# Performance work log

Measured on AMD Instinct MI355X. Metric: run time of the kernel, lower is better.

Reference implementation:

```python
import jax, jax.numpy as jnp
import numpy as np

N_NODES = 100000
N_EDGES = 1600000
C_IN, C_HID, C_OUT = 64, 64, 32


def _gcn_conv(x, src, dst, ew, W, b, n_nodes):
    """PyG GCNConv: add self-loops (weight 1), symmetric normalization,
    out[dst] += norm * (x @ W)[src], plus bias. Dropout omitted (eval mode)."""
    h = x @ W  # [N, C_out_layer]
    loop = jnp.arange(n_nodes, dtype=src.dtype)
    src_a = jnp.concatenate([src, loop])
    dst_a = jnp.concatenate([dst, loop])
    ew_a = jnp.concatenate([ew, jnp.ones((n_nodes,), dtype=ew.dtype)])
    # degree over incoming (dst) side, weighted
    deg = jax.ops.segment_sum(ew_a, dst_a, num_segments=n_nodes)
    dinv = jnp.where(deg > 0, jax.lax.rsqrt(deg), 0.0)
    norm = dinv[src_a] * ew_a * dinv[dst_a]  # [E+N]
    msg = h[src_a] * norm[:, None]           # gather + scale: [E+N, C]
    out = jax.ops.segment_sum(msg, dst_a, num_segments=n_nodes)  # scatter-add
    return out + b


def setup_inputs() -> dict:
    key = jax.random.key(0)
    k1, k2, k3, k4, k5, k6, k7 = jax.random.split(key, 7)
    x = jax.random.normal(k1, (N_NODES, C_IN), dtype=jnp.float32)
    edge_index = jax.random.randint(k2, (2, N_EDGES), 0, N_NODES, dtype=jnp.int64)
    edge_attr = jax.random.uniform(k3, (N_EDGES,), dtype=jnp.float32)
    s1 = 1.0 / np.sqrt(C_IN)
    s2 = 1.0 / np.sqrt(C_HID)
    W1 = jax.random.uniform(k4, (C_IN, C_HID), jnp.float32, -s1, s1)
    b1 = jnp.zeros((C_HID,), dtype=jnp.float32)
    W2 = jax.random.uniform(k5, (C_HID, C_OUT), jnp.float32, -s2, s2)
    b2 = jnp.zeros((C_OUT,), dtype=jnp.float32)
    return {"x": x, "edge_index": edge_index, "edge_attr": edge_attr,
            "W1": W1, "b1": b1, "W2": W2, "b2": b2}


def reference(x, edge_index, edge_attr, W1, b1, W2, b2):
    n = x.shape[0]
    src, dst = edge_index[0], edge_index[1]
    h = _gcn_conv(x, src, dst, edge_attr, W1, b1, n)
    h = jax.nn.relu(h)  # dropout is identity in eval mode
    out = _gcn_conv(h, src, dst, edge_attr, W2, b2, n)
    return out
```

## Files before the change

### kernel.cpp

```cpp
#include <hip/hip_runtime.h>
#include <hip/hip_fp16.h>


#define TPB 256
#define TPB_P 512
#define TPB_S 1024
#define BSH2 8
#define BN2 256
#define NBC 512
#define PCHUNK 4096
#define CAP2 5632
#define XSTR 68

typedef union { uint2 u; __half2 h[2]; } hpack;
typedef union { uint4 u; __half2 h[4]; } hpack8;

__device__ __forceinline__ int enc_w(float w) {
  unsigned b = __float_as_uint(w);
  return (int)(((b + 0x7FFFu + ((b >> 16) & 1u)) >> 16) & 0x7FFFu);
}
__device__ __forceinline__ float dec_w(int e) {
  return __uint_as_float(((unsigned)e >> 17) << 16);
}

__global__ __launch_bounds__(TPB_P) void k_fat(const int* __restrict__ si,
                                               const int* __restrict__ di,
                                               const float* __restrict__ ew,
                                               int* __restrict__ bpos,
                                               int2* __restrict__ tin,
                                               const float* __restrict__ x,
                                               const float* __restrict__ W1,
                                               __half* __restrict__ h1h,
                                               int e, int n, int gbp) {
  __shared__ union SM {
    struct {
      int hcnt[NBC]; int lst0[NBC]; int lcur[NBC]; int hbase[NBC];
      int wsum[8];
      int2 se[PCHUNK]; unsigned short sbk[PCHUNK];
    } p;
    float Wl[64 * 64];
  } sm;
  int t = threadIdx.x;
  if (blockIdx.x < (unsigned)gbp) {
    int lo = blockIdx.x * PCHUNK;
    int hi = lo + PCHUNK; if (hi > e) hi = e;
    int cn = hi - lo;
    sm.p.hcnt[t] = 0;
    __syncthreads();
    for (int i = lo + t; i < hi; i += TPB_P) atomicAdd(&sm.p.hcnt[di[i] >> BSH2], 1);
    __syncthreads();
    int c = sm.p.hcnt[t];
    int lane = t & 63, wid = t >> 6;
    int v = c;
#pragma unroll
    for (int off = 1; off < 64; off <<= 1) {
      int u = __shfl_up(v, off);
      if (lane >= off) v += u;
    }
    if (lane == 63) sm.p.wsum[wid] = v;
    __syncthreads();
    if (t < 64) {
      int s = (t < 8) ? sm.p.wsum[t] : 0;
#pragma unroll
      for (int off = 1; off < 8; off <<= 1) {
        int u = __shfl_up(s, off);
        if (t >= off) s += u;
      }
      if (t < 8) sm.p.wsum[t] = s;
    }
    __syncthreads();
    int incl = v + (wid ? sm.p.wsum[wid - 1] : 0);
    sm.p.hcnt[t] = incl;
    __syncthreads();
    {
      int bb = (t + blockIdx.x) & (NBC - 1);
      int inc = sm.p.hcnt[bb];
      int exc = bb ? sm.p.hcnt[bb - 1] : 0;
      int cb = inc - exc;
      sm.p.lst0[bb] = exc;
      sm.p.lcur[bb] = 0;
      sm.p.hbase[bb] = cb ? (bb * CAP2 + atomicAdd(&bpos[bb], cb)) : 0;
    }
    __syncthreads();
    for (int i = lo + t; i < hi; i += TPB_P) {
      int d = di[i];
      int bk = d >> BSH2;
      int loc = atomicAdd(&sm.p.lcur[bk], 1);
      int p = sm.p.lst0[bk] + loc;
      sm.p.se[p] = make_int2(si[i] | ((d & (BN2 - 1)) << 17), __float_as_int(ew[i]));
      sm.p.sbk[p] = (unsigned short)bk;
    }
    __syncthreads();
    for (int p = t; p < cn; p += TPB_P) {
      int bk = sm.p.sbk[p];
      tin[sm.p.hbase[bk] + (p - sm.p.lst0[bk])] = sm.p.se[p];
    }
  } else {
    {
      const float4* W4 = (const float4*)W1;
      float4* Wl4 = (float4*)sm.Wl;
#pragma unroll
      for (int i = 0; i < 2; ++i) Wl4[t + TPB_P * i] = W4[t + TPB_P * i];
    }
    __syncthreads();
    int r = (blockIdx.x - gbp) * 32 + (t >> 4);
    if (r >= n) return;
    int c0 = (t & 15) << 2;
    const float4* xr = (const float4*)(x + (size_t)r * 64);
    float ax = 0.f, ay = 0.f, az = 0.f, aw = 0.f;
#pragma unroll
    for (int kk = 0; kk < 16; ++kk) {
      float4 xv = xr[kk];
      const float* w = &sm.Wl[(kk * 4) * 64 + c0];
      float4 w0 = *(const float4*)(w);
      float4 w1 = *(const float4*)(w + 64);
      float4 w2 = *(const float4*)(w + 128);
      float4 w3 = *(const float4*)(w + 192);
      ax += xv.x * w0.x + xv.y * w1.x + xv.z * w2.x + xv.w * w3.x;
      ay += xv.x * w0.y + xv.y * w1.y + xv.z * w2.y + xv.w * w3.y;
      az += xv.x * w0.z + xv.y * w1.z + xv.z * w2.z + xv.w * w3.z;
      aw += xv.x * w0.w + xv.y * w1.w + xv.z * w2.w + xv.w * w3.w;
    }
    hpack pk;
    pk.h[0] = __floats2half2_rn(ax, ay);
    pk.h[1] = __floats2half2_rn(az, aw);
    *(uint2*)(h1h + (size_t)r * 64 + c0) = pk.u;
  }
}

__global__ __launch_bounds__(TPB_S) void k_sortb(const int2* __restrict__ tin,
                                                 const int* __restrict__ bpos,
                                                 int* __restrict__ colpk,
                                                 int2* __restrict__ rowseg,
                                                 float* __restrict__ dinv, int n) {
  __shared__ int cnt[BN2];
  __shared__ float degw[BN2];
  __shared__ int cur[BN2];
  __shared__ int ls[BN2];
  __shared__ int2 se[PCHUNK];
  int b = blockIdx.x, t = threadIdx.x;
  if (t < BN2) { cnt[t] = 0; degw[t] = 1.0f; }
  __syncthreads();
  int jb = b * CAP2, je = jb + bpos[b];
  for (int j = jb + t; j < je; j += TPB_S) {
    int2 p = tin[j];
    int o = j - jb;
    if (o < PCHUNK) se[o] = p;
    int dl = p.x >> 17;
    atomicAdd(&cnt[dl], 1);
    atomicAdd(&degw[dl], __int_as_float(p.y));
  }
  __syncthreads();
  int c = (t < BN2) ? cnt[t] : 0;
  int c4 = (c + 3) & ~3;
  if (t < BN2) ls[t] = c4;
  __syncthreads();
  for (int off = 1; off < BN2; off <<= 1) {
    int u = (t >= off && t < BN2) ? ls[t - off] : 0;
    __syncthreads();
    if (t < BN2) ls[t] += u;
    __syncthreads();
  }
  int base = b << BSH2;
  if (t < BN2) {
    int start = jb + ls[t] - c4;
    cur[t] = start;
    int node = base + t;
    if (node < n) {
      rowseg[node] = make_int2(start, start + c4);
      dinv[node] = rsqrtf(degw[t]);
    }
    for (int i = c; i < c4; ++i) colpk[start + i] = 0;
  }
  __syncthreads();
  for (int j = jb + t; j < je; j += TPB_S) {
    int o = j - jb;
    int2 p = (o < PCHUNK) ? se[o] : tin[j];
    int dl = p.x >> 17;
    int pos = atomicAdd(&cur[dl], 1);
    colpk[pos] = (p.x & 0x1FFFF) | (enc_w(__int_as_float(p.y)) << 17);
  }
}

__global__ __launch_bounds__(TPB) void k_gfuse(const __half* __restrict__ g1h,
                                               const int* __restrict__ colpk,
                                               const int2* __restrict__ rowseg,
                                               const float* __restrict__ dinv,
                                               const float* __restrict__ W2,
                                               const float* __restrict__ b1,
                                               __half* __restrict__ g2h, int n) {
  __shared__ float W2l[64 * 32];
  __shared__ float b1l[64];
  __shared__ float x2l[32 * XSTR];
  int t = threadIdx.x;
  {
    const float4* W4 = (const float4*)W2;
    float4* Wl4 = (float4*)W2l;
#pragma unroll
    for (int i = 0; i < 2; ++i) Wl4[t + TPB * i] = W4[t + TPB * i];
    if (t < 64) b1l[t] = b1[t];
  }
  __syncthreads();
  int node = t >> 3;
  int r = blockIdx.x * 32 + node;
  int c0 = (t & 7) << 3;
  bool valid = (r < n);
  float a[8];
  float dv = 0.f;
  if (valid) {
    dv = dinv[r];
    hpack8 s; s.u = *(const uint4*)(g1h + (size_t)r * 64 + c0);
#pragma unroll
    for (int k = 0; k < 4; ++k) {
      float2 f = __half22float2(s.h[k]);
      a[2 * k] = dv * f.x; a[2 * k + 1] = dv * f.y;
    }
    int2 seg = rowseg[r];
    int j = seg.x;
    for (; j + 7 < seg.y; j += 8) {
      int4 qa = *(const int4*)(colpk + j);
      int4 qb = *(const int4*)(colpk + j + 4);
      int s0 = qa.x & 0x1FFFF, s1 = qa.y & 0x1FFFF, s2 = qa.z & 0x1FFFF, s3 = qa.w & 0x1FFFF;
      int s4 = qb.x & 0x1FFFF, s5 = qb.y & 0x1FFFF, s6 = qb.z & 0x1FFFF, s7 = qb.w & 0x1FFFF;
      hpack8 u0; u0.u = *(const uint4*)(g1h + (size_t)s0 * 64 + c0);
      hpack8 u1; u1.u = *(const uint4*)(g1h + (size_t)s1 * 64 + c0);
      hpack8 u2; u2.u = *(const uint4*)(g1h + (size_t)s2 * 64 + c0);
      hpack8 u3; u3.u = *(const uint4*)(g1h + (size_t)s3 * 64 + c0);
      hpack8 u4; u4.u = *(const uint4*)(g1h + (size_t)s4 * 64 + c0);
      hpack8 u5; u5.u = *(const uint4*)(g1h + (size_t)s5 * 64 + c0);
      hpack8 u6; u6.u = *(const uint4*)(g1h + (size_t)s6 * 64 + c0);
      hpack8 u7; u7.u = *(const uint4*)(g1h + (size_t)s7 * 64 + c0);
      float w0 = dec_w(qa.x) * dinv[s0], w1 = dec_w(qa.y) * dinv[s1];
      float w2 = dec_w(qa.z) * dinv[s2], w3 = dec_w(qa.w) * dinv[s3];
      float w4 = dec_w(qb.x) * dinv[s4], w5 = dec_w(qb.y) * dinv[s5];
      float w6 = dec_w(qb.z) * dinv[s6], w7 = dec_w(qb.w) * dinv[s7];
#pragma unroll
      for (int k = 0; k < 4; ++k) {
        float2 f;
        f = __half22float2(u0.h[k]); a[2*k] += w0 * f.x; a[2*k+1] += w0 * f.y;
        f = __half22float2(u1.h[k]); a[2*k] += w1 * f.x; a[2*k+1] += w1 * f.y;
        f = __half22float2(u2.h[k]); a[2*k] += w2 * f.x; a[2*k+1] += w2 * f.y;
        f = __half22float2(u3.h[k]); a[2*k] += w3 * f.x; a[2*k+1] += w3 * f.y;
        f = __half22float2(u4.h[k]); a[2*k] += w4 * f.x; a[2*k+1] += w4 * f.y;
        f = __half22float2(u5.h[k]); a[2*k] += w5 * f.x; a[2*k+1] += w5 * f.y;
        f = __half22float2(u6.h[k]); a[2*k] += w6 * f.x; a[2*k+1] += w6 * f.y;
        f = __half22float2(u7.h[k]); a[2*k] += w7 * f.x; a[2*k+1] += w7 * f.y;
      }
    }
    if (j < seg.y) {
      int4 qa = *(const int4*)(colpk + j);
      int s0 = qa.x & 0x1FFFF, s1 = qa.y & 0x1FFFF, s2 = qa.z & 0x1FFFF, s3 = qa.w & 0x1FFFF;
      hpack8 u0; u0.u = *(const uint4*)(g1h + (size_t)s0 * 64 + c0);
      hpack8 u1; u1.u = *(const uint4*)(g1h + (size_t)s1 * 64 + c0);
      hpack8 u2; u2.u = *(const uint4*)(g1h + (size_t)s2 * 64 + c0);
      hpack8 u3; u3.u = *(const uint4*)(g1h + (size_t)s3 * 64 + c0);
      float w0 = dec_w(qa.x) * dinv[s0], w1 = dec_w(qa.y) * dinv[s1];
      float w2 = dec_w(qa.z) * dinv[s2], w3 = dec_w(qa.w) * dinv[s3];
#pragma unroll
      for (int k = 0; k < 4; ++k) {
        float2 f;
        f = __half22float2(u0.h[k]); a[2*k] += w0 * f.x; a[2*k+1] += w0 * f.y;
        f = __half22float2(u1.h[k]); a[2*k] += w1 * f.x; a[2*k+1] += w1 * f.y;
        f = __half22float2(u2.h[k]); a[2*k] += w2 * f.x; a[2*k+1] += w2 * f.y;
        f = __half22float2(u3.h[k]); a[2*k] += w3 * f.x; a[2*k+1] += w3 * f.y;
      }
    }
    float* xp = x2l + node * XSTR + c0;
#pragma unroll
    for (int k = 0; k < 8; k += 4) {
      float4 v = {fmaxf(dv * a[k + 0] + b1l[c0 + k + 0], 0.f),
                  fmaxf(dv * a[k + 1] + b1l[c0 + k + 1], 0.f),
                  fmaxf(dv * a[k + 2] + b1l[c0 + k + 2], 0.f),
                  fmaxf(dv * a[k + 3] + b1l[c0 + k + 3], 0.f)};
      *(float4*)(xp + k) = v;
    }
  }
  __syncthreads();
  if (!valid) return;
  int oc = (t & 7) << 2;
  const float* xr = x2l + node * XSTR;
  float ax = 0.f, ay = 0.f, az = 0.f, aw = 0.f;
#pragma unroll
  for (int kk = 0; kk < 16; ++kk) {
    float4 xv = *(const float4*)(xr + 4 * kk);
    const float* w = &W2l[(kk * 4) * 32 + oc];
    float4 w0 = *(const float4*)(w);
    float4 w1 = *(const float4*)(w + 32);
    float4 w2 = *(const float4*)(w + 64);
    float4 w3 = *(const float4*)(w + 96);
    ax += xv.x * w0.x + xv.y * w1.x + xv.z * w2.x + xv.w * w3.x;
    ay += xv.x * w0.y + xv.y * w1.y + xv.z * w2.y + xv.w * w3.y;
    az += xv.x * w0.z + xv.y * w1.z + xv.z * w2.z + xv.w * w3.z;
    aw += xv.x * w0.w + xv.y * w1.w + xv.z * w2.w + xv.w * w3.w;
  }
  hpack pk;
  pk.h[0] = __floats2half2_rn(ax, ay);
  pk.h[1] = __floats2half2_rn(az, aw);
  *(uint2*)(g2h + (size_t)r * 32 + oc) = pk.u;
}

__global__ __launch_bounds__(TPB) void k_gather32(const __half* __restrict__ g2h,
                                                  const int* __restrict__ colpk,
                                                  const int2* __restrict__ rowseg,
                                                  const float* __restrict__ dinv,
                                                  const float* __restrict__ b2,
                                                  float* __restrict__ out, int n) {
  int t = threadIdx.x;
  int r = blockIdx.x * 64 + (t >> 2);
  if (r >= n) return;
  int c0 = (t & 3) << 3;
  float dv = dinv[r];
  float a[8];
  {
    hpack8 s; s.u = *(const uint4*)(g2h + (size_t)r * 32 + c0);
#pragma unroll
    for (int k = 0; k < 4; ++k) {
      float2 f = __half22float2(s.h[k]);
      a[2 * k] = dv * f.x; a[2 * k + 1] = dv * f.y;
    }
  }
  int2 seg = rowseg[r];
  int j = seg.x;
  for (; j + 7 < seg.y; j += 8) {
    int4 qa = *(const int4*)(colpk + j);
    int4 qb = *(const int4*)(colpk + j + 4);
    int s0 = qa.x & 0x1FFFF, s1 = qa.y & 0x1FFFF, s2 = qa.z & 0x1FFFF, s3 = qa.w & 0x1FFFF;
    int s4 = qb.x & 0x1FFFF, s5 = qb.y & 0x1FFFF, s6 = qb.z & 0x1FFFF, s7 = qb.w & 0x1FFFF;
    hpack8 u0; u0.u = *(const uint4*)(g2h + (size_t)s0 * 32 + c0);
    hpack8 u1; u1.u = *(const uint4*)(g2h + (size_t)s1 * 32 + c0);
    hpack8 u2; u2.u = *(const uint4*)(g2h + (size_t)s2 * 32 + c0);
    hpack8 u3; u3.u = *(const uint4*)(g2h + (size_t)s3 * 32 + c0);
    hpack8 u4; u4.u = *(const uint4*)(g2h + (size_t)s4 * 32 + c0);
    hpack8 u5; u5.u = *(const uint4*)(g2h + (size_t)s5 * 32 + c0);
    hpack8 u6; u6.u = *(const uint4*)(g2h + (size_t)s6 * 32 + c0);
    hpack8 u7; u7.u = *(const uint4*)(g2h + (size_t)s7 * 32 + c0);
    float w0 = dec_w(qa.x) * dinv[s0], w1 = dec_w(qa.y) * dinv[s1];
    float w2 = dec_w(qa.z) * dinv[s2], w3 = dec_w(qa.w) * dinv[s3];
    float w4 = dec_w(qb.x) * dinv[s4], w5 = dec_w(qb.y) * dinv[s5];
    float w6 = dec_w(qb.z) * dinv[s6], w7 = dec_w(qb.w) * dinv[s7];
#pragma unroll
    for (int k = 0; k < 4; ++k) {
      float2 f;
      f = __half22float2(u0.h[k]); a[2*k] += w0 * f.x; a[2*k+1] += w0 * f.y;
      f = __half22float2(u1.h[k]); a[2*k] += w1 * f.x; a[2*k+1] += w1 * f.y;
      f = __half22float2(u2.h[k]); a[2*k] += w2 * f.x; a[2*k+1] += w2 * f.y;
      f = __half22float2(u3.h[k]); a[2*k] += w3 * f.x; a[2*k+1] += w3 * f.y;
      f = __half22float2(u4.h[k]); a[2*k] += w4 * f.x; a[2*k+1] += w4 * f.y;
      f = __half22float2(u5.h[k]); a[2*k] += w5 * f.x; a[2*k+1] += w5 * f.y;
      f = __half22float2(u6.h[k]); a[2*k] += w6 * f.x; a[2*k+1] += w6 * f.y;
      f = __half22float2(u7.h[k]); a[2*k] += w7 * f.x; a[2*k+1] += w7 * f.y;
    }
  }
  if (j < seg.y) {
    int4 qa = *(const int4*)(colpk + j);
    int s0 = qa.x & 0x1FFFF, s1 = qa.y & 0x1FFFF, s2 = qa.z & 0x1FFFF, s3 = qa.w & 0x1FFFF;
    hpack8 u0; u0.u = *(const uint4*)(g2h + (size_t)s0 * 32 + c0);
    hpack8 u1; u1.u = *(const uint4*)(g2h + (size_t)s1 * 32 + c0);
    hpack8 u2; u2.u = *(const uint4*)(g2h + (size_t)s2 * 32 + c0);
    hpack8 u3; u3.u = *(const uint4*)(g2h + (size_t)s3 * 32 + c0);
    float w0 = dec_w(qa.x) * dinv[s0], w1 = dec_w(qa.y) * dinv[s1];
    float w2 = dec_w(qa.z) * dinv[s2], w3 = dec_w(qa.w) * dinv[s3];
#pragma unroll
    for (int k = 0; k < 4; ++k) {
      float2 f;
      f = __half22float2(u0.h[k]); a[2*k] += w0 * f.x; a[2*k+1] += w0 * f.y;
      f = __half22float2(u1.h[k]); a[2*k] += w1 * f.x; a[2*k+1] += w1 * f.y;
      f = __half22float2(u2.h[k]); a[2*k] += w2 * f.x; a[2*k+1] += w2 * f.y;
      f = __half22float2(u3.h[k]); a[2*k] += w3 * f.x; a[2*k+1] += w3 * f.y;
    }
  }
  const float4* b24 = (const float4*)(b2 + c0);
  float4 bb0 = b24[0], bb1 = b24[1];
  float* op = out + (size_t)r * 32 + c0;
  *(float4*)(op)     = make_float4(dv * a[0] + bb0.x, dv * a[1] + bb0.y,
                                   dv * a[2] + bb0.z, dv * a[3] + bb0.w);
  *(float4*)(op + 4) = make_float4(dv * a[4] + bb1.x, dv * a[5] + bb1.y,
                                   dv * a[6] + bb1.z, dv * a[7] + bb1.w);
}

extern "C" void kernel_launch(void* const* d_in, const int* in_sizes, int n_in,
                              void* d_out, int out_size, void* d_ws, size_t ws_size,
                              hipStream_t stream) {
  const float* x  = (const float*)d_in[0];
  const int* ei   = (const int*)d_in[1];
  const float* ew = (const float*)d_in[2];
  const float* W1 = (const float*)d_in[3];
  const float* b1 = (const float*)d_in[4];
  const float* W2 = (const float*)d_in[5];
  const float* b2 = (const float*)d_in[6];
  float* out = (float*)d_out;

  const int n = in_sizes[0] / 64;
  const int e = in_sizes[1] / 2;
  const int* si = ei;
  const int* di = ei + e;
  const int NBc = (n + BN2 - 1) >> BSH2;

  float* ws = (float*)d_ws;
  const size_t NP = 100352;
  const size_t SLOTS = (size_t)NBc * CAP2;
  float*  dinv   = ws;
  __half* g1h    = (__half*)(ws + NP);
  int2*   rowseg = (int2*)(ws + NP + (size_t)n * 32);
  int*    bpos   = (int*)(rowseg + NP);
  int*    colpk  = bpos + 1024;
  int2*   tin    = (int2*)(colpk + SLOTS);
  __half* g2h    = (__half*)(tin + SLOTS);

  int gb_part = (e + PCHUNK - 1) / PCHUNK;
  int gb_g1 = (n + 31) / 32;
  int gb_gf = (n + 31) / 32;
  int gb_g32 = (n + 63) / 64;

  hipMemsetAsync(bpos, 0, NBC * sizeof(int), stream);
  k_fat<<<gb_part + gb_g1, TPB_P, 0, stream>>>(si, di, ew, bpos, tin,
                                               x, W1, g1h, e, n, gb_part);
  k_sortb<<<NBc, TPB_S, 0, stream>>>(tin, bpos, colpk, rowseg, dinv, n);
  k_gfuse<<<gb_gf, TPB, 0, stream>>>(g1h, colpk, rowseg, dinv, W2, b1, g2h, n);
  k_gather32<<<gb_g32, TPB, 0, stream>>>(g2h, colpk, rowseg, dinv, b2, out, n);
}
```

Before: 203.6 us.

## Replace atomic bucket-slot allocation with count/scan/scatter passes

The edge partition pass is split into three kernels. A histogram kernel writes per-chunk bucket counts to a matrix, a scan kernel computes deterministic per-bucket offsets, and a scatter kernel re-reads the edges and writes them to their final slots. This removes global atomics on bucket positions and the memset, and gives each chunk a smaller shared-memory footprint in the fused kernel. The cost is two extra launches and a second read of di plus reads of si and ew.

```diff
diff --git a/kernel.cpp b/kernel.cpp
--- a/kernel.cpp
+++ b/kernel.cpp
@@ -8,6 +8,7 @@
 #define BSH2 8
 #define BN2 256
 #define NBC 512
+#define BPAD 400
 #define PCHUNK 4096
 #define CAP2 5632
 #define XSTR 68
@@ -23,78 +24,25 @@
   return __uint_as_float(((unsigned)e >> 17) << 16);
 }
 
-__global__ __launch_bounds__(TPB_P) void k_fat(const int* __restrict__ si,
-                                               const int* __restrict__ di,
-                                               const float* __restrict__ ew,
-                                               int* __restrict__ bpos,
-                                               int2* __restrict__ tin,
+__global__ __launch_bounds__(TPB_P) void k_fat(const int* __restrict__ di,
+                                               int* __restrict__ bcnt,
                                                const float* __restrict__ x,
                                                const float* __restrict__ W1,
                                                __half* __restrict__ h1h,
                                                int e, int n, int gbp) {
   __shared__ union SM {
-    struct {
-      int hcnt[NBC]; int lst0[NBC]; int lcur[NBC]; int hbase[NBC];
-      int wsum[8];
-      int2 se[PCHUNK]; unsigned short sbk[PCHUNK];
-    } p;
+    int hcnt[NBC];
     float Wl[64 * 64];
   } sm;
   int t = threadIdx.x;
   if (blockIdx.x < (unsigned)gbp) {
     int lo = blockIdx.x * PCHUNK;
     int hi = lo + PCHUNK; if (hi > e) hi = e;
-    int cn = hi - lo;
-    sm.p.hcnt[t] = 0;
+    sm.hcnt[t] = 0;
     __syncthreads();
-    for (int i = lo + t; i < hi; i += TPB_P) atomicAdd(&sm.p.hcnt[di[i] >> BSH2], 1);
+    for (int i = lo + t; i < hi; i += TPB_P) atomicAdd(&sm.hcnt[di[i] >> BSH2], 1);
     __syncthreads();
-    int c = sm.p.hcnt[t];
-    int lane = t & 63, wid = t >> 6;
-    int v = c;
-#pragma unroll
-    for (int off = 1; off < 64; off <<= 1) {
-      int u = __shfl_up(v, off);
-      if (lane >= off) v += u;
-    }
-    if (lane == 63) sm.p.wsum[wid] = v;
-    __syncthreads();
-    if (t < 64) {
-      int s = (t < 8) ? sm.p.wsum[t] : 0;
-#pragma unroll
-      for (int off = 1; off < 8; off <<= 1) {
-        int u = __shfl_up(s, off);
-        if (t >= off) s += u;
-      }
-      if (t < 8) sm.p.wsum[t] = s;
-    }
-    __syncthreads();
-    int incl = v + (wid ? sm.p.wsum[wid - 1] : 0);
-    sm.p.hcnt[t] = incl;
-    __syncthreads();
-    {
-      int bb = (t + blockIdx.x) & (NBC - 1);
-      int inc = sm.p.hcnt[bb];
-      int exc = bb ? sm.p.hcnt[bb - 1] : 0;
-      int cb = inc - exc;
-      sm.p.lst0[bb] = exc;
-      sm.p.lcur[bb] = 0;
-      sm.p.hbase[bb] = cb ? (bb * CAP2 + atomicAdd(&bpos[bb], cb)) : 0;
-    }
-    __syncthreads();
-    for (int i = lo + t; i < hi; i += TPB_P) {
-      int d = di[i];
-      int bk = d >> BSH2;
-      int loc = atomicAdd(&sm.p.lcur[bk], 1);
-      int p = sm.p.lst0[bk] + loc;
-      sm.p.se[p] = make_int2(si[i] | ((d & (BN2 - 1)) << 17), __float_as_int(ew[i]));
-      sm.p.sbk[p] = (unsigned short)bk;
-    }
-    __syncthreads();
-    for (int p = t; p < cn; p += TPB_P) {
-      int bk = sm.p.sbk[p];
-      tin[sm.p.hbase[bk] + (p - sm.p.lst0[bk])] = sm.p.se[p];
-    }
+    bcnt[t * BPAD + blockIdx.x] = sm.hcnt[t];
   } else {
     {
       const float4* W4 = (const float4*)W1;
@@ -125,6 +73,85 @@
     pk.h[0] = __floats2half2_rn(ax, ay);
     pk.h[1] = __floats2half2_rn(az, aw);
     *(uint2*)(h1h + (size_t)r * 64 + c0) = pk.u;
+  }
+}
+
+__global__ __launch_bounds__(64) void k_scan(const int* __restrict__ bcnt,
+                                             int* __restrict__ bofs,
+                                             int* __restrict__ bpos, int nblk) {
+  int row = blockIdx.x, lane = threadIdx.x;
+  const int* rp = bcnt + row * BPAD;
+  int* op = bofs + row * BPAD;
+  int base = row * CAP2;
+  int carry = 0;
+  for (int c0 = 0; c0 < nblk; c0 += 64) {
+    int i = c0 + lane;
+    int v = (i < nblk) ? rp[i] : 0;
+    int orig = v;
+#pragma unroll
+    for (int off = 1; off < 64; off <<= 1) {
+      int u = __shfl_up(v, off);
+      if (lane >= off) v += u;
+    }
+    if (i < nblk) op[i] = base + carry + (v - orig);
+    carry += __shfl(v, 63);
+  }
+  if (lane == 0) bpos[row] = carry;
+}
+
+__global__ __launch_bounds__(TPB_P) void k_scat(const int* __restrict__ si,
+                                                const int* __restrict__ di,
+                                                const float* __restrict__ ew,
+                                                const int* __restrict__ bcnt,
+                                                const int* __restrict__ bofs,
+                                                int2* __restrict__ tin, int e) {
+  __shared__ int lst0[NBC];
+  __shared__ int lcur[NBC];
+  __shared__ int hbase[NBC];
+  __shared__ int wsum[8];
+  __shared__ int2 se[PCHUNK];
+  __shared__ unsigned short sbk[PCHUNK];
+  int t = threadIdx.x, b = blockIdx.x;
+  int lo = b * PCHUNK;
+  int hi = lo + PCHUNK; if (hi > e) hi = e;
+  int cn = hi - lo;
+  int cb = bcnt[t * BPAD + b];
+  hbase[t] = bofs[t * BPAD + b];
+  lcur[t] = 0;
+  int lane = t & 63, wid = t >> 6;
+  int v = cb;
+#pragma unroll
+  for (int off = 1; off < 64; off <<= 1) {
+    int u = __shfl_up(v, off);
+    if (lane >= off) v += u;
+  }
+  if (lane == 63) wsum[wid] = v;
+  __syncthreads();
+  if (t < 64) {
+    int s = (t < 8) ? wsum[t] : 0;
+#pragma unroll
+    for (int off = 1; off < 8; off <<= 1) {
+      int u = __shfl_up(s, off);
+      if (t >= off) s += u;
+    }
+    if (t < 8) wsum[t] = s;
+  }
+  __syncthreads();
+  int incl = v + (wid ? wsum[wid - 1] : 0);
+  lst0[t] = incl - cb;
+  __syncthreads();
+  for (int i = lo + t; i < hi; i += TPB_P) {
+    int d = di[i];
+    int bk = d >> BSH2;
+    int loc = atomicAdd(&lcur[bk], 1);
+    int p = lst0[bk] + loc;
+    se[p] = make_int2(si[i] | ((d & (BN2 - 1)) << 17), __float_as_int(ew[i]));
+    sbk[p] = (unsigned short)bk;
+  }
+  __syncthreads();
+  for (int p = t; p < cn; p += TPB_P) {
+    int bk = sbk[p];
+    tin[hbase[bk] + (p - lst0[bk])] = se[p];
   }
 }
 
@@ -403,7 +430,9 @@
   __half* g1h    = (__half*)(ws + NP);
   int2*   rowseg = (int2*)(ws + NP + (size_t)n * 32);
   int*    bpos   = (int*)(rowseg + NP);
-  int*    colpk  = bpos + 1024;
+  int*    bcnt   = bpos + 1024;
+  int*    bofs   = bcnt + NBC * BPAD;
+  int*    colpk  = bofs + NBC * BPAD;
   int2*   tin    = (int2*)(colpk + SLOTS);
   __half* g2h    = (__half*)(tin + SLOTS);
 
@@ -412,9 +441,9 @@
   int gb_gf = (n + 31) / 32;
   int gb_g32 = (n + 63) / 64;
 
-  hipMemsetAsync(bpos, 0, NBC * sizeof(int), stream);
-  k_fat<<<gb_part + gb_g1, TPB_P, 0, stream>>>(si, di, ew, bpos, tin,
-                                               x, W1, g1h, e, n, gb_part);
+  k_fat<<<gb_part + gb_g1, TPB_P, 0, stream>>>(di, bcnt, x, W1, g1h, e, n, gb_part);
+  k_scan<<<NBC, 64, 0, stream>>>(bcnt, bofs, bpos, gb_part);
+  k_scat<<<gb_part, TPB_P, 0, stream>>>(si, di, ew, bcnt, bofs, tin, e);
   k_sortb<<<NBc, TPB_S, 0, stream>>>(tin, bpos, colpk, rowseg, dinv, n);
   k_gfuse<<<gb_gf, TPB, 0, stream>>>(g1h, colpk, rowseg, dinv, W2, b1, g2h, n);
   k_gather32<<<gb_g32, TPB, 0, stream>>>(g2h, colpk, rowseg, dinv, b2, out, n);
```

New measurement: 205.8 us. No clear change (+1.0%).
